# Kernel optimization log

Measured on AMD Instinct MI355X. Metric: run time of the kernel, lower is better.

Reference implementation:

```python
import jax, jax.numpy as jnp
import numpy as np

ALPHA = 0.0005
TAU = 0.2


def setup_inputs() -> dict:
    key = jax.random.key(0)
    k1, k2, k3 = jax.random.split(key, 3)
    x_batch = jax.random.normal(k1, (2048, 4096), dtype=jnp.float32)
    y_batch = jax.random.normal(k2, (2048, 4096), dtype=jnp.float32)
    # conv weight [out_ch, in_ch, kh, kw]; sliced along dim 2 (F = 64)
    conv_w = jax.random.normal(k3, (512, 512, 64, 3), dtype=jnp.float32) * 0.05
    return {"x_batch": x_batch, "y_batch": y_batch, "conv_w": conv_w}


def _diversity_reg(conv_w, tau):
    # slices conv_w[:, :, i, :] flattened -> rows of v: [F, out*in*kw]
    F = conv_w.shape[2]
    v = jnp.transpose(conv_w, (2, 0, 1, 3)).reshape(F, -1)
    norms = jnp.sqrt(jnp.sum(v * v, axis=1))  # [F]
    gram = v @ v.T  # [F, F] -- memory-bound tall-skinny reduction
    sim = gram / (norms[:, None] * norms[None, :])
    eye = jnp.eye(F, dtype=bool)
    # keep iff tau < sim <= 1 and i != j; zeroed entries are detached (constant 0)
    mask = (sim > tau) & (sim <= 1.0) & (~eye)
    return jnp.sum(jnp.where(mask, sim, 0.0))


def reference(x_batch, y_batch, conv_w):
    # loss_function = MSELoss (mean reduction)
    loss_value = jnp.mean((x_batch - y_batch) ** 2)
    reg_value = _diversity_reg(conv_w, TAU)
    return loss_value + ALPHA * reg_value
```

## Files before the change

kernel.cpp:

```cpp
#include <hip/hip_runtime.h>

typedef __attribute__((ext_vector_type(8)))  short   short8;
typedef __attribute__((ext_vector_type(4)))  unsigned uint4v;
typedef __attribute__((ext_vector_type(16))) float   f32x16;

constexpr int GRAM_BLOCKS = 256;
constexpr int MSE_BLOCKS  = 256;
constexpr int BLOCK       = 256;
constexpr int SLAB_F      = 192;
constexpr int CHUNK_SLABS = 16;
constexpr int CHUNK_F     = CHUNK_SLABS * SLAB_F;
constexpr int NSLAB       = 512 * 512;
constexpr int NCHUNK      = NSLAB / CHUNK_SLABS;
constexpr int GRAM_WAVES  = GRAM_BLOCKS * (BLOCK / 64);
constexpr int CHUNKS_PER_WAVE = NCHUNK / GRAM_WAVES;
constexpr unsigned MSE_N4 = 2097152u;
constexpr int MSE_THREADS = MSE_BLOCKS * BLOCK;


struct F3 { float v[3]; };
struct Chunk { F3 a0[4], a1[4], b0[4], b1[4]; };

__device__ __forceinline__ unsigned pk_bf16(float a, float b) {
  unsigned a2 = __builtin_bit_cast(unsigned, a) + 0x8000u;
  unsigned b2 = __builtin_bit_cast(unsigned, b) + 0x8000u;
  return __builtin_amdgcn_perm(b2, a2, 0x07060302u);
}

__device__ __forceinline__ void load_chunk(const float* __restrict__ s, int laneoff,
                                           Chunk& c) {
#pragma unroll
  for (int bp = 0; bp < 4; ++bp) {
    const float* p = s + laneoff + bp * 384;
    c.a0[bp] = *(const F3*)(p);
    c.a1[bp] = *(const F3*)(p + 96);
    c.b0[bp] = *(const F3*)(p + 192);
    c.b1[bp] = *(const F3*)(p + 288);
  }
}

__device__ __forceinline__ void mac_chunk(const Chunk& c, f32x16& a00, f32x16& a01,
                                          f32x16& a11) {
#pragma unroll
  for (int k = 0; k < 3; ++k) {
    unsigned fl[4], fh[4];
#pragma unroll
    for (int bp = 0; bp < 4; ++bp) {
      fl[bp] = pk_bf16(c.a0[bp].v[k], c.b0[bp].v[k]);
      fh[bp] = pk_bf16(c.a1[bp].v[k], c.b1[bp].v[k]);
    }
    uint4v vl = {fl[0], fl[1], fl[2], fl[3]};
    uint4v vh = {fh[0], fh[1], fh[2], fh[3]};
    short8 lo = __builtin_bit_cast(short8, vl);
    short8 hv = __builtin_bit_cast(short8, vh);
    a00 = __builtin_amdgcn_mfma_f32_32x32x16_bf16(lo, lo, a00, 0, 0, 0);
    a01 = __builtin_amdgcn_mfma_f32_32x32x16_bf16(lo, hv, a01, 0, 0, 0);
    a11 = __builtin_amdgcn_mfma_f32_32x32x16_bf16(hv, hv, a11, 0, 0, 0);
  }
}

__global__ __launch_bounds__(BLOCK, 2) void k_main(
    const float* __restrict__ X, const float* __restrict__ Y,
    const float* __restrict__ W, float* __restrict__ ws) {
  __shared__ float red[2][3072];
  const int bid = blockIdx.x;
  const int tid = threadIdx.x;

  if (bid >= GRAM_BLOCKS) {
    const int t0 = (bid - GRAM_BLOCKS) * BLOCK + tid;
    const float4* x4 = (const float4*)X;
    const float4* y4 = (const float4*)Y;
    float acc = 0.f;
    for (unsigned i = (unsigned)t0; i < MSE_N4; i += (unsigned)MSE_THREADS) {
      float4 a = x4[i], b = y4[i];
      float d0 = a.x - b.x, d1 = a.y - b.y, d2 = a.z - b.z, d3 = a.w - b.w;
      acc += d0 * d0 + d1 * d1 + d2 * d2 + d3 * d3;
    }
#pragma unroll
    for (int o = 32; o; o >>= 1) acc += __shfl_xor(acc, o, 64);
    if ((tid & 63) == 0) atomicAdd(&ws[0], acc);
    return;
  }

  const int wave = tid >> 6;
  const int lane = tid & 63;
  const int r    = lane & 31;
  const int hi   = lane >> 5;
  const int wg   = bid * 4 + wave;
  const int laneoff = hi * 1536 + 3 * r;
  const float* base = W + (size_t)(wg * CHUNKS_PER_WAVE) * CHUNK_F;

  f32x16 a00{}, a01{}, a11{};
  Chunk ca, cb;
  load_chunk(base, laneoff, ca);
#pragma unroll
  for (int t = 0; t < CHUNKS_PER_WAVE; t += 2) {
    load_chunk(base + (t + 1) * CHUNK_F, laneoff, cb);
    mac_chunk(ca, a00, a01, a11);
    if (t + 2 < CHUNKS_PER_WAVE) load_chunk(base + (t + 2) * CHUNK_F, laneoff, ca);
    mac_chunk(cb, a00, a01, a11);
  }

  if (wave < 2) {
#pragma unroll
    for (int rg = 0; rg < 16; ++rg) {
      red[wave][       rg * 64 + lane] = a00[rg];
      red[wave][1024 + rg * 64 + lane] = a01[rg];
      red[wave][2048 + rg * 64 + lane] = a11[rg];
    }
  }
  __syncthreads();
  if (wave >= 2) {
    float* dst = red[wave - 2];
#pragma unroll
    for (int rg = 0; rg < 16; ++rg) {
      dst[       rg * 64 + lane] += a00[rg];
      dst[1024 + rg * 64 + lane] += a01[rg];
      dst[2048 + rg * 64 + lane] += a11[rg];
    }
  }
  __syncthreads();
  float* gram = ws + 64;
  for (int e = tid; e < 3072; e += BLOCK)
    atomicAdd(&gram[e], red[0][e] + red[1][e]);
}

__global__ __launch_bounds__(256) void k_fin(const float* __restrict__ ws,
                                             float* __restrict__ out) {
  __shared__ float g[3072];
  __shared__ float n2[64];
  __shared__ float wsum[4];
  const int tid = threadIdx.x;

  for (int e = tid; e < 3072; e += 256) g[e] = ws[64 + e];
  __syncthreads();

  for (int e = tid; e < 3072; e += 256) {
    int tl = e >> 10, rg = (e >> 6) & 15, l = e & 63;
    int il = (rg & 3) + 8 * (rg >> 2) + 4 * (l >> 5);
    int jl = l & 31;
    if (tl != 1 && il == jl) n2[il + (tl == 2 ? 32 : 0)] = g[e];
  }
  __syncthreads();

  float local = 0.f;
  for (int e = tid; e < 3072; e += 256) {
    int tl = e >> 10, rg = (e >> 6) & 15, l = e & 63;
    int il = (rg & 3) + 8 * (rg >> 2) + 4 * (l >> 5);
    int jl = l & 31;
    int i, j; float wgt;
    if (tl == 0)      { i = il;      j = jl;      wgt = 1.f; }
    else if (tl == 1) { i = il;      j = jl + 32; wgt = 2.f; }
    else              { i = il + 32; j = jl + 32; wgt = 1.f; }
    if (i != j) {
      float sim = g[e] / sqrtf(n2[i] * n2[j]);
      if (sim > 0.2f && sim <= 1.0f) local += wgt * sim;
    }
  }
#pragma unroll
  for (int o = 32; o; o >>= 1) local += __shfl_xor(local, o, 64);
  if ((tid & 63) == 0) wsum[tid >> 6] = local;
  __syncthreads();
  if (tid == 0) {
    float reg_sum = wsum[0] + wsum[1] + wsum[2] + wsum[3];
    out[0] = ws[0] * (1.0f / 8388608.0f) + 0.0005f * reg_sum;
  }
}

extern "C" void kernel_launch(void* const* d_in, const int* in_sizes, int n_in,
                              void* d_out, int out_size, void* d_ws, size_t ws_size,
                              hipStream_t stream) {
  const float* X = (const float*)d_in[0];
  const float* Y = (const float*)d_in[1];
  const float* W = (const float*)d_in[2];
  float* ws = (float*)d_ws;

  hipMemsetAsync(d_ws, 0, (64 + 3072) * sizeof(float), stream);
  k_main<<<GRAM_BLOCKS + MSE_BLOCKS, BLOCK, 0, stream>>>(X, Y, W, ws);
  k_fin<<<1, 256, 0, stream>>>(ws, (float*)d_out);
}
```

Before: 64.34 us.

## Rebalance gram/MSE blocks, stride gram chunks, and slice gram atomics

Shifts the block split toward the gram reduction (384 gram vs 128 MSE blocks) and has each wave step through chunks with a stride of the total wave count instead of owning one contiguous range, which handles the uneven chunk count. Gram partials are spread over 8 atomic slices to reduce atomic contention, and MSE partials are written per block without atomics, then summed in the finalize kernel. The aim is better balance of the conv_w and x/y streams and less atomic serialization, in exchange for a larger memset and extra reads in k_fin.

```diff
diff --git a/kernel.cpp b/kernel.cpp
--- a/kernel.cpp
+++ b/kernel.cpp
@@ -4,16 +4,14 @@
 typedef __attribute__((ext_vector_type(4)))  unsigned uint4v;
 typedef __attribute__((ext_vector_type(16))) float   f32x16;
 
-constexpr int GRAM_BLOCKS = 256;
-constexpr int MSE_BLOCKS  = 256;
+constexpr int GRAM_BLOCKS = 384;
+constexpr int MSE_BLOCKS  = 128;
 constexpr int BLOCK       = 256;
 constexpr int SLAB_F      = 192;
-constexpr int CHUNK_SLABS = 16;
-constexpr int CHUNK_F     = CHUNK_SLABS * SLAB_F;
-constexpr int NSLAB       = 512 * 512;
-constexpr int NCHUNK      = NSLAB / CHUNK_SLABS;
-constexpr int GRAM_WAVES  = GRAM_BLOCKS * (BLOCK / 64);
-constexpr int CHUNKS_PER_WAVE = NCHUNK / GRAM_WAVES;
+constexpr int CHUNK_F     = 3072;
+constexpr int NCHUNK      = 16384;
+constexpr int GRAM_WAVES  = GRAM_BLOCKS * 4;
+constexpr int NSLICE      = 8;
 constexpr unsigned MSE_N4 = 2097152u;
 constexpr int MSE_THREADS = MSE_BLOCKS * BLOCK;
 
@@ -27,15 +25,16 @@
   return __builtin_amdgcn_perm(b2, a2, 0x07060302u);
 }
 
-__device__ __forceinline__ void load_chunk(const float* __restrict__ s, int laneoff,
-                                           Chunk& c) {
+__device__ __forceinline__ void load_chunk(const float* __restrict__ W, int c,
+                                           int laneoff, Chunk& ch) {
+  const float* s = W + (size_t)c * CHUNK_F + laneoff;
 #pragma unroll
   for (int bp = 0; bp < 4; ++bp) {
-    const float* p = s + laneoff + bp * 384;
-    c.a0[bp] = *(const F3*)(p);
-    c.a1[bp] = *(const F3*)(p + 96);
-    c.b0[bp] = *(const F3*)(p + 192);
-    c.b1[bp] = *(const F3*)(p + 288);
+    const float* p = s + bp * 384;
+    ch.a0[bp] = *(const F3*)(p);
+    ch.a1[bp] = *(const F3*)(p + 96);
+    ch.b0[bp] = *(const F3*)(p + 192);
+    ch.b1[bp] = *(const F3*)(p + 288);
   }
 }
 
@@ -65,40 +64,49 @@
   __shared__ float red[2][3072];
   const int bid = blockIdx.x;
   const int tid = threadIdx.x;
+  const int wave = tid >> 6;
+  const int lane = tid & 63;
 
   if (bid >= GRAM_BLOCKS) {
-    const int t0 = (bid - GRAM_BLOCKS) * BLOCK + tid;
+    const unsigned t0 = (unsigned)((bid - GRAM_BLOCKS) * BLOCK + tid);
     const float4* x4 = (const float4*)X;
     const float4* y4 = (const float4*)Y;
     float acc = 0.f;
-    for (unsigned i = (unsigned)t0; i < MSE_N4; i += (unsigned)MSE_THREADS) {
+#pragma unroll 8
+    for (int it = 0; it < 64; ++it) {
+      unsigned i = t0 + (unsigned)it * (unsigned)MSE_THREADS;
       float4 a = x4[i], b = y4[i];
       float d0 = a.x - b.x, d1 = a.y - b.y, d2 = a.z - b.z, d3 = a.w - b.w;
       acc += d0 * d0 + d1 * d1 + d2 * d2 + d3 * d3;
     }
 #pragma unroll
     for (int o = 32; o; o >>= 1) acc += __shfl_xor(acc, o, 64);
-    if ((tid & 63) == 0) atomicAdd(&ws[0], acc);
+    __shared__ float wsum[4];
+    if (lane == 0) wsum[wave] = acc;
+    __syncthreads();
+    if (tid == 0) ws[bid - GRAM_BLOCKS] = wsum[0] + wsum[1] + wsum[2] + wsum[3];
     return;
   }
 
-  const int wave = tid >> 6;
-  const int lane = tid & 63;
   const int r    = lane & 31;
   const int hi   = lane >> 5;
-  const int wg   = bid * 4 + wave;
   const int laneoff = hi * 1536 + 3 * r;
-  const float* base = W + (size_t)(wg * CHUNKS_PER_WAVE) * CHUNK_F;
+  const int wg = bid * 4 + wave;
 
   f32x16 a00{}, a01{}, a11{};
   Chunk ca, cb;
-  load_chunk(base, laneoff, ca);
-#pragma unroll
-  for (int t = 0; t < CHUNKS_PER_WAVE; t += 2) {
-    load_chunk(base + (t + 1) * CHUNK_F, laneoff, cb);
+  int c = wg;
+  load_chunk(W, c, laneoff, ca);
+  c += GRAM_WAVES;
+  for (;;) {
+    if (c < NCHUNK) load_chunk(W, c, laneoff, cb);
     mac_chunk(ca, a00, a01, a11);
-    if (t + 2 < CHUNKS_PER_WAVE) load_chunk(base + (t + 2) * CHUNK_F, laneoff, ca);
+    if (c >= NCHUNK) break;
+    c += GRAM_WAVES;
+    if (c < NCHUNK) load_chunk(W, c, laneoff, ca);
     mac_chunk(cb, a00, a01, a11);
+    if (c >= NCHUNK) break;
+    c += GRAM_WAVES;
   }
 
   if (wave < 2) {
@@ -120,9 +128,9 @@
     }
   }
   __syncthreads();
-  float* gram = ws + 64;
+  float* slice = ws + 128 + (bid & (NSLICE - 1)) * 3072;
   for (int e = tid; e < 3072; e += BLOCK)
-    atomicAdd(&gram[e], red[0][e] + red[1][e]);
+    atomicAdd(&slice[e], red[0][e] + red[1][e]);
 }
 
 __global__ __launch_bounds__(256) void k_fin(const float* __restrict__ ws,
@@ -130,9 +138,20 @@
   __shared__ float g[3072];
   __shared__ float n2[64];
   __shared__ float wsum[4];
+  __shared__ float msum_s[4];
   const int tid = threadIdx.x;
-
-  for (int e = tid; e < 3072; e += 256) g[e] = ws[64 + e];
+  const int wave = tid >> 6, lane = tid & 63;
+
+  for (int e = tid; e < 3072; e += 256) {
+    float s = 0.f;
+#pragma unroll
+    for (int sl = 0; sl < NSLICE; ++sl) s += ws[128 + sl * 3072 + e];
+    g[e] = s;
+  }
+  float m = (tid < 128) ? ws[tid] : 0.f;
+#pragma unroll
+  for (int o = 32; o; o >>= 1) m += __shfl_xor(m, o, 64);
+  if (lane == 0) msum_s[wave] = m;
   __syncthreads();
 
   for (int e = tid; e < 3072; e += 256) {
@@ -159,11 +178,12 @@
   }
 #pragma unroll
   for (int o = 32; o; o >>= 1) local += __shfl_xor(local, o, 64);
-  if ((tid & 63) == 0) wsum[tid >> 6] = local;
+  if (lane == 0) wsum[wave] = local;
   __syncthreads();
   if (tid == 0) {
     float reg_sum = wsum[0] + wsum[1] + wsum[2] + wsum[3];
-    out[0] = ws[0] * (1.0f / 8388608.0f) + 0.0005f * reg_sum;
+    float mse_sum = msum_s[0] + msum_s[1] + msum_s[2] + msum_s[3];
+    out[0] = mse_sum * (1.0f / 8388608.0f) + 0.0005f * reg_sum;
   }
 }
 
@@ -175,7 +195,8 @@
   const float* W = (const float*)d_in[2];
   float* ws = (float*)d_ws;
 
-  hipMemsetAsync(d_ws, 0, (64 + 3072) * sizeof(float), stream);
+  hipMemsetAsync((void*)((char*)d_ws + 128 * sizeof(float)), 0,
+                 NSLICE * 3072 * sizeof(float), stream);
   k_main<<<GRAM_BLOCKS + MSE_BLOCKS, BLOCK, 0, stream>>>(X, Y, W, ws);
   k_fin<<<1, 256, 0, stream>>>(ws, (float*)d_out);
 }
```

After: 65.24 us. No clear change (+1.4%).
